# Kernel optimization log

Hardware: AMD Instinct MI355X
Metric: run time of the kernel (lower is better)

The kernel has to match this reference:

```python
import jax, jax.numpy as jnp
import numpy as np


def _sage_layer(x, neighbors, W, b):
    # x: (N, D), neighbors: (N, deg) int indices into x
    neigh_agg = x[neighbors].mean(axis=1)           # (N, D) gather + mean
    h = jnp.concatenate([x, neigh_agg], axis=-1)     # (N, 2D)
    return jax.nn.relu(h @ W + b)                    # (N, D_out)


def setup_inputs() -> dict:
    key = jax.random.key(0)
    k1, k2, k3, k4 = jax.random.split(key, 4)
    N, D, DEG = 50000, 128, 16
    x = jax.random.normal(k1, (N, D), dtype=jnp.float32)
    neighbors = jax.random.randint(k2, (N, DEG), 0, N)
    # Linear(in_dim*2, out_dim) weights, stored as (2D, D_out) for x @ W
    scale = 1.0 / np.sqrt(2 * D)
    W1 = jax.random.normal(k3, (2 * D, D), dtype=jnp.float32) * scale
    b1 = jnp.zeros((D,), dtype=jnp.float32)
    W2 = jax.random.normal(k4, (2 * D, D), dtype=jnp.float32) * scale
    b2 = jnp.zeros((D,), dtype=jnp.float32)
    return {"x": x, "neighbors": neighbors, "W1": W1, "b1": b1, "W2": W2, "b2": b2}


def reference(x, neighbors, W1, b1, W2, b2):
    h = _sage_layer(x, neighbors, W1, b1)
    h = _sage_layer(h, neighbors, W2, b2)
    return h
```

## Files before the change

kernel.cpp:

```cpp
#include <hip/hip_runtime.h>

typedef __attribute__((ext_vector_type(8))) short short8;
typedef __attribute__((ext_vector_type(4))) float f32x4;
typedef __attribute__((ext_vector_type(2))) float f32x2;

#define N_NODES 50000
#define D 128
#define DEG 16
#define K2 256
#define BM 64

static __device__ __forceinline__ unsigned short f2b(float f) {
    union { float f; unsigned int u; } v; v.f = f;
    return (unsigned short)((v.u + 0x7fffu + ((v.u >> 16) & 1u)) >> 16);
}

__global__ void prep(const float* __restrict__ x, unsigned short* __restrict__ xb,
                     const float* __restrict__ W1, const float* __restrict__ W2,
                     unsigned short* __restrict__ Wf1, unsigned short* __restrict__ Wf2) {
    int b = blockIdx.x;
    if (b < 32) {
        int o  = (b * 256 + threadIdx.x) * 4;
        int e0 = o & 7;
        int l  = (o >> 3) & 63;
        int ct = (o >> 9) & 1;
        int kk = (o >> 10) & 7;
        int w  = o >> 13;
        int n  = w * 32 + ((l & 15) << 1) + ct;
        int kb = kk * 32 + (l >> 4) * 8 + e0;
        ushort4 a, c;
        a.x = f2b(W1[(kb + 0) * D + n]);
        a.y = f2b(W1[(kb + 1) * D + n]);
        a.z = f2b(W1[(kb + 2) * D + n]);
        a.w = f2b(W1[(kb + 3) * D + n]);
        *(ushort4*)(Wf1 + o) = a;
        c.x = f2b(W2[(kb + 0) * D + n]);
        c.y = f2b(W2[(kb + 1) * D + n]);
        c.z = f2b(W2[(kb + 2) * D + n]);
        c.w = f2b(W2[(kb + 3) * D + n]);
        *(ushort4*)(Wf2 + o) = c;
    } else {
        int i = ((b - 32) * 256 + threadIdx.x) * 4;
        if (i < N_NODES * D) {
            float4 v = *(const float4*)(x + i);
            ushort4 o4;
            o4.x = f2b(v.x); o4.y = f2b(v.y); o4.z = f2b(v.z); o4.w = f2b(v.w);
            *(ushort4*)(xb + i) = o4;
        }
    }
}

template <int OUT_BF16>
__global__ __launch_bounds__(256, 3)
void sage_layer(const unsigned short* __restrict__ feat,
                const int* __restrict__ nbr,
                const unsigned short* __restrict__ wf,
                const float* __restrict__ bias,
                void* __restrict__ out)
{
    __shared__ __align__(16) unsigned short Hl[BM * 264];
    __shared__ int Nl[BM * DEG];
    const int tid  = threadIdx.x;
    const int row0 = blockIdx.x * BM;

    {
        int g = row0 * DEG + tid * 4;
        int gmax = N_NODES * DEG - 4;
        if (g > gmax) g = gmax;
        *(int4*)(Nl + tid * 4) = *(const int4*)(nbr + g);
    }
    __syncthreads();

    const char* fb = (const char*)feat;

    #pragma unroll
    for (int p = 0; p < 4; ++p) {
        int a = tid + p * 256;
        int r = a >> 4;
        int s = a & 15;
        int grow = row0 + r;
        if (grow >= N_NODES) grow = N_NODES - 1;
        unsigned sB = (unsigned)s * 16u;
        short8 self = *(const short8*)(fb + (unsigned)grow * 256u + sB);

        int4 i0 = *(const int4*)(Nl + r * 16);
        int4 i1 = *(const int4*)(Nl + r * 16 + 4);
        int4 i2 = *(const int4*)(Nl + r * 16 + 8);
        int4 i3 = *(const int4*)(Nl + r * 16 + 12);
        int ids[16] = { i0.x, i0.y, i0.z, i0.w, i1.x, i1.y, i1.z, i1.w,
                        i2.x, i2.y, i2.z, i2.w, i3.x, i3.y, i3.z, i3.w };

        short8 v[16];
        #pragma unroll
        for (int j = 0; j < 16; ++j)
            v[j] = *(const short8*)(fb + (((unsigned)ids[j]) << 8) + sB);

        f32x2 am[4];
        #pragma unroll
        for (int i = 0; i < 4; ++i) am[i] = (f32x2){0.f, 0.f};
        #pragma unroll
        for (int j = 0; j < 16; ++j) {
            union { short8 s8; unsigned u[4]; } vv; vv.s8 = v[j];
            #pragma unroll
            for (int i = 0; i < 4; ++i) {
                unsigned ui = vv.u[i];
                f32x2 e;
                e.x = __uint_as_float(ui << 16);
                e.y = __uint_as_float(ui & 0xffff0000u);
                am[i] += e;
            }
        }

        unsigned short* hr = Hl + r * 264 + s * 8;
        *(short8*)(hr) = self;
        union { unsigned short u[8]; short8 s8; } m;
        #pragma unroll
        for (int i = 0; i < 4; ++i) {
            m.u[2 * i]     = f2b(am[i].x * 0.0625f);
            m.u[2 * i + 1] = f2b(am[i].y * 0.0625f);
        }
        *(short8*)(hr + D) = m.s8;
    }

    const int lane = tid & 63;
    const int w    = tid >> 6;
    const int quad = lane >> 4;
    const int l16  = lane & 15;
    const int n_base = w * 32;
    const unsigned short* wfw = wf + w * 8192;
    short8 bfrag[8][2];
    #pragma unroll
    for (int kk = 0; kk < 8; ++kk)
        #pragma unroll
        for (int ct = 0; ct < 2; ++ct)
            bfrag[kk][ct] = *(const short8*)(wfw + kk * 1024 + ct * 512 + lane * 8);

    __syncthreads();

    f32x4 acc[4][2];
    #pragma unroll
    for (int rt = 0; rt < 4; ++rt)
        #pragma unroll
        for (int ct = 0; ct < 2; ++ct)
            acc[rt][ct] = (f32x4){0.f, 0.f, 0.f, 0.f};

    #pragma unroll
    for (int kk = 0; kk < 8; ++kk) {
        short8 afrag[4];
        #pragma unroll
        for (int rt = 0; rt < 4; ++rt)
            afrag[rt] = *(const short8*)(&Hl[(rt * 16 + l16) * 264 + kk * 32 + quad * 8]);
        #pragma unroll
        for (int rt = 0; rt < 4; ++rt)
            #pragma unroll
            for (int ct = 0; ct < 2; ++ct)
                acc[rt][ct] = __builtin_amdgcn_mfma_f32_16x16x32_bf16(
                    afrag[rt], bfrag[kk][ct], acc[rt][ct], 0, 0, 0);
    }

    const int col0 = n_base + (l16 << 1);
    float2 bv = *(const float2*)(bias + col0);
    #pragma unroll
    for (int rt = 0; rt < 4; ++rt) {
        int grow_base = row0 + rt * 16 + quad * 4;
        #pragma unroll
        for (int r = 0; r < 4; ++r) {
            int grow = grow_base + r;
            if (grow >= N_NODES) continue;
            float v0 = acc[rt][0][r] + bv.x;
            float v1 = acc[rt][1][r] + bv.y;
            v0 = v0 > 0.f ? v0 : 0.f;
            v1 = v1 > 0.f ? v1 : 0.f;
            if (OUT_BF16) {
                unsigned u = (unsigned)f2b(v0) | ((unsigned)f2b(v1) << 16);
                *(unsigned*)((unsigned short*)out + grow * D + col0) = u;
            } else {
                float2 o2; o2.x = v0; o2.y = v1;
                *(float2*)((float*)out + grow * D + col0) = o2;
            }
        }
    }
}

extern "C" void kernel_launch(void* const* d_in, const int* in_sizes, int n_in,
                              void* d_out, int out_size, void* d_ws, size_t ws_size,
                              hipStream_t stream) {
    const float* x  = (const float*)d_in[0];
    const int*   nb = (const int*)d_in[1];
    const float* W1 = (const float*)d_in[2];
    const float* b1 = (const float*)d_in[3];
    const float* W2 = (const float*)d_in[4];
    const float* b2 = (const float*)d_in[5];

    char* ws = (char*)d_ws;
    unsigned short* Wf1 = (unsigned short*)(ws);
    unsigned short* Wf2 = (unsigned short*)(ws + 65536);
    unsigned short* xb  = (unsigned short*)(ws + 131072);
    unsigned short* h1  = (unsigned short*)(ws + 131072 + 12800000);

    prep<<<32 + 6250, 256, 0, stream>>>(x, xb, W1, W2, Wf1, Wf2);

    const int mgrid = (N_NODES + BM - 1) / BM;
    sage_layer<1><<<mgrid, 256, 0, stream>>>(xb, nb, Wf1, b1, h1);
    sage_layer<0><<<mgrid, 256, 0, stream>>>(h1, nb, Wf2, b2, d_out);
}
```

Before: 147.8 us.

## Split fused SAGE layer into column-chunked gather and LDS-swizzled GEMM kernels

Stores bf16 features in a column-chunked layout: four chunks of 32 features each, one 64-byte row segment per node per chunk. Each layer is split into a separate gather-mean kernel, run with a chunk dimension in the grid so the random gathers in one pass touch a smaller working set, and a GEMM kernel. The GEMM loads A tiles straight into swizzled LDS with global_load_lds. This aims to improve cache locality of the random neighbor gathers and raise occupancy. The cost is two extra kernel launches and a round trip through global memory for the mean buffer.

```diff
diff --git a/kernel.cpp b/kernel.cpp
--- a/kernel.cpp
+++ b/kernel.cpp
@@ -8,14 +8,14 @@
 #define D 128
 #define DEG 16
 #define K2 256
-#define BM 64
+#define CHSZ (N_NODES * 64u)
 
 static __device__ __forceinline__ unsigned short f2b(float f) {
     union { float f; unsigned int u; } v; v.f = f;
     return (unsigned short)((v.u + 0x7fffu + ((v.u >> 16) & 1u)) >> 16);
 }
 
-__global__ void prep(const float* __restrict__ x, unsigned short* __restrict__ xb,
+__global__ void prep(const float* __restrict__ x, unsigned short* __restrict__ xcm,
                      const float* __restrict__ W1, const float* __restrict__ W2,
                      unsigned short* __restrict__ Wf1, unsigned short* __restrict__ Wf2) {
     int b = blockIdx.x;
@@ -40,94 +40,116 @@
         c.w = f2b(W2[(kb + 3) * D + n]);
         *(ushort4*)(Wf2 + o) = c;
     } else {
-        int i = ((b - 32) * 256 + threadIdx.x) * 4;
-        if (i < N_NODES * D) {
-            float4 v = *(const float4*)(x + i);
-            ushort4 o4;
-            o4.x = f2b(v.x); o4.y = f2b(v.y); o4.z = f2b(v.z); o4.w = f2b(v.w);
-            *(ushort4*)(xb + i) = o4;
-        }
-    }
-}
-
-template <int OUT_BF16>
-__global__ __launch_bounds__(256, 3)
-void sage_layer(const unsigned short* __restrict__ feat,
-                const int* __restrict__ nbr,
-                const unsigned short* __restrict__ wf,
-                const float* __restrict__ bias,
-                void* __restrict__ out)
+        unsigned o = ((unsigned)(b - 32) * 256u + threadIdx.x) * 16u;
+        unsigned rowidx = o >> 6;
+        unsigned c = rowidx / N_NODES;
+        unsigned n = rowidx - c * N_NODES;
+        unsigned d0 = (o & 63u) >> 1;
+        const float* src = x + n * 128 + c * 32 + d0;
+        float4 v0 = *(const float4*)src;
+        float4 v1 = *(const float4*)(src + 4);
+        union { unsigned short u[8]; short8 s8; } m;
+        m.u[0] = f2b(v0.x); m.u[1] = f2b(v0.y); m.u[2] = f2b(v0.z); m.u[3] = f2b(v0.w);
+        m.u[4] = f2b(v1.x); m.u[5] = f2b(v1.y); m.u[6] = f2b(v1.z); m.u[7] = f2b(v1.w);
+        *(short8*)((char*)xcm + o) = m.s8;
+    }
+}
+
+__global__ __launch_bounds__(256, 4)
+void gather_mean(const unsigned short* __restrict__ fcm,
+                 const int* __restrict__ nbr,
+                 unsigned short* __restrict__ Mcm)
 {
-    __shared__ __align__(16) unsigned short Hl[BM * 264];
-    __shared__ int Nl[BM * DEG];
+    __shared__ __align__(16) int Nl[1024];
     const int tid  = threadIdx.x;
-    const int row0 = blockIdx.x * BM;
-
-    {
-        int g = row0 * DEG + tid * 4;
-        int gmax = N_NODES * DEG - 4;
-        if (g > gmax) g = gmax;
-        *(int4*)(Nl + tid * 4) = *(const int4*)(nbr + g);
-    }
+    const int row0 = blockIdx.x * 64;
+    const char* base = (const char*)fcm + blockIdx.y * CHSZ;
+
+    int g = row0 * DEG + tid * 4;
+    int gmax = N_NODES * DEG - 4;
+    if (g > gmax) g = gmax;
+    *(int4*)(Nl + tid * 4) = *(const int4*)(nbr + g);
     __syncthreads();
 
-    const char* fb = (const char*)feat;
-
-    #pragma unroll
-    for (int p = 0; p < 4; ++p) {
-        int a = tid + p * 256;
-        int r = a >> 4;
-        int s = a & 15;
-        int grow = row0 + r;
-        if (grow >= N_NODES) grow = N_NODES - 1;
-        unsigned sB = (unsigned)s * 16u;
-        short8 self = *(const short8*)(fb + (unsigned)grow * 256u + sB);
-
-        int4 i0 = *(const int4*)(Nl + r * 16);
-        int4 i1 = *(const int4*)(Nl + r * 16 + 4);
-        int4 i2 = *(const int4*)(Nl + r * 16 + 8);
-        int4 i3 = *(const int4*)(Nl + r * 16 + 12);
-        int ids[16] = { i0.x, i0.y, i0.z, i0.w, i1.x, i1.y, i1.z, i1.w,
-                        i2.x, i2.y, i2.z, i2.w, i3.x, i3.y, i3.z, i3.w };
-
-        short8 v[16];
-        #pragma unroll
-        for (int j = 0; j < 16; ++j)
-            v[j] = *(const short8*)(fb + (((unsigned)ids[j]) << 8) + sB);
-
-        f32x2 am[4];
-        #pragma unroll
-        for (int i = 0; i < 4; ++i) am[i] = (f32x2){0.f, 0.f};
-        #pragma unroll
-        for (int j = 0; j < 16; ++j) {
-            union { short8 s8; unsigned u[4]; } vv; vv.s8 = v[j];
-            #pragma unroll
-            for (int i = 0; i < 4; ++i) {
-                unsigned ui = vv.u[i];
-                f32x2 e;
-                e.x = __uint_as_float(ui << 16);
-                e.y = __uint_as_float(ui & 0xffff0000u);
-                am[i] += e;
-            }
-        }
-
-        unsigned short* hr = Hl + r * 264 + s * 8;
-        *(short8*)(hr) = self;
+    const int r = tid >> 2, s = tid & 3;
+    const int grow = row0 + r;
+    const unsigned sB = (unsigned)s * 16u;
+
+    int4 i0 = *(const int4*)(Nl + r * 16);
+    int4 i1 = *(const int4*)(Nl + r * 16 + 4);
+    int4 i2 = *(const int4*)(Nl + r * 16 + 8);
+    int4 i3 = *(const int4*)(Nl + r * 16 + 12);
+    int ids[16] = { i0.x, i0.y, i0.z, i0.w, i1.x, i1.y, i1.z, i1.w,
+                    i2.x, i2.y, i2.z, i2.w, i3.x, i3.y, i3.z, i3.w };
+
+    short8 v[16];
+    #pragma unroll
+    for (int j = 0; j < 16; ++j)
+        v[j] = *(const short8*)(base + (((unsigned)ids[j]) << 6) + sB);
+
+    f32x2 am[4];
+    #pragma unroll
+    for (int i = 0; i < 4; ++i) am[i] = (f32x2){0.f, 0.f};
+    #pragma unroll
+    for (int j = 0; j < 16; ++j) {
+        union { short8 s8; unsigned u[4]; } vv; vv.s8 = v[j];
+        #pragma unroll
+        for (int i = 0; i < 4; ++i) {
+            unsigned ui = vv.u[i];
+            f32x2 e;
+            e.x = __uint_as_float(ui << 16);
+            e.y = __uint_as_float(ui & 0xffff0000u);
+            am[i] += e;
+        }
+    }
+
+    if (grow < N_NODES) {
         union { unsigned short u[8]; short8 s8; } m;
         #pragma unroll
         for (int i = 0; i < 4; ++i) {
             m.u[2 * i]     = f2b(am[i].x * 0.0625f);
             m.u[2 * i + 1] = f2b(am[i].y * 0.0625f);
         }
-        *(short8*)(hr + D) = m.s8;
-    }
-
+        *(short8*)((char*)Mcm + blockIdx.y * CHSZ + (unsigned)grow * 64u + sB) = m.s8;
+    }
+}
+
+template <int OUT_F32>
+__global__ __launch_bounds__(256, 4)
+void gemm(const unsigned short* __restrict__ fcm,
+          const unsigned short* __restrict__ Mcm,
+          const unsigned short* __restrict__ wf,
+          const float* __restrict__ bias,
+          void* __restrict__ out)
+{
+    __shared__ __align__(16) char Al[32 * 512];
+    const int tid  = threadIdx.x;
+    const int row0 = blockIdx.x * 32;
+    const int wave = tid >> 6;
     const int lane = tid & 63;
-    const int w    = tid >> 6;
     const int quad = lane >> 4;
     const int l16  = lane & 15;
-    const int n_base = w * 32;
-    const unsigned short* wfw = wf + w * 8192;
+
+    #pragma unroll
+    for (int i = 0; i < 4; ++i) {
+        unsigned o    = (unsigned)i * 4096u + (unsigned)tid * 16u;
+        unsigned row  = o >> 9;
+        unsigned colb = o & 511u;
+        unsigned scol = colb ^ ((row & 7u) << 4);
+        int grow = row0 + (int)row;
+        if (grow >= N_NODES) grow = N_NODES - 1;
+        const unsigned short* buf = (scol < 256u) ? fcm : Mcm;
+        unsigned cb = scol & 255u;
+        const char* src = (const char*)buf + (cb >> 6) * CHSZ
+                          + (unsigned)grow * 64u + (cb & 63u);
+        __builtin_amdgcn_global_load_lds(
+            (const __attribute__((address_space(1))) unsigned int*)src,
+            (__attribute__((address_space(3))) unsigned int*)
+                (Al + i * 4096 + wave * 1024),
+            16, 0, 0);
+    }
+
+    const unsigned short* wfw = wf + wave * 8192;
     short8 bfrag[8][2];
     #pragma unroll
     for (int kk = 0; kk < 8; ++kk)
@@ -137,46 +159,51 @@
 
     __syncthreads();
 
-    f32x4 acc[4][2];
-    #pragma unroll
-    for (int rt = 0; rt < 4; ++rt)
+    f32x4 acc[2][2];
+    #pragma unroll
+    for (int rt = 0; rt < 2; ++rt)
         #pragma unroll
         for (int ct = 0; ct < 2; ++ct)
             acc[rt][ct] = (f32x4){0.f, 0.f, 0.f, 0.f};
 
     #pragma unroll
     for (int kk = 0; kk < 8; ++kk) {
-        short8 afrag[4];
-        #pragma unroll
-        for (int rt = 0; rt < 4; ++rt)
-            afrag[rt] = *(const short8*)(&Hl[(rt * 16 + l16) * 264 + kk * 32 + quad * 8]);
-        #pragma unroll
-        for (int rt = 0; rt < 4; ++rt)
+        short8 af[2];
+        #pragma unroll
+        for (int rt = 0; rt < 2; ++rt) {
+            unsigned row  = (unsigned)(rt * 16 + l16);
+            unsigned byte = row * 512u + (unsigned)kk * 64u + (unsigned)quad * 16u;
+            byte ^= (row & 7u) << 4;
+            af[rt] = *(const short8*)(Al + byte);
+        }
+        #pragma unroll
+        for (int rt = 0; rt < 2; ++rt)
             #pragma unroll
             for (int ct = 0; ct < 2; ++ct)
                 acc[rt][ct] = __builtin_amdgcn_mfma_f32_16x16x32_bf16(
-                    afrag[rt], bfrag[kk][ct], acc[rt][ct], 0, 0, 0);
-    }
-
-    const int col0 = n_base + (l16 << 1);
+                    af[rt], bfrag[kk][ct], acc[rt][ct], 0, 0, 0);
+    }
+
+    const int col0 = wave * 32 + (l16 << 1);
     float2 bv = *(const float2*)(bias + col0);
     #pragma unroll
-    for (int rt = 0; rt < 4; ++rt) {
-        int grow_base = row0 + rt * 16 + quad * 4;
+    for (int rt = 0; rt < 2; ++rt) {
+        int gb = row0 + rt * 16 + quad * 4;
         #pragma unroll
         for (int r = 0; r < 4; ++r) {
-            int grow = grow_base + r;
+            int grow = gb + r;
             if (grow >= N_NODES) continue;
             float v0 = acc[rt][0][r] + bv.x;
             float v1 = acc[rt][1][r] + bv.y;
             v0 = v0 > 0.f ? v0 : 0.f;
             v1 = v1 > 0.f ? v1 : 0.f;
-            if (OUT_BF16) {
+            if (OUT_F32) {
+                f32x2 o2; o2.x = v0; o2.y = v1;
+                *(f32x2*)((float*)out + grow * D + col0) = o2;
+            } else {
                 unsigned u = (unsigned)f2b(v0) | ((unsigned)f2b(v1) << 16);
-                *(unsigned*)((unsigned short*)out + grow * D + col0) = u;
-            } else {
-                float2 o2; o2.x = v0; o2.y = v1;
-                *(float2*)((float*)out + grow * D + col0) = o2;
+                *(unsigned*)((char*)out + (col0 >> 5) * CHSZ
+                             + (unsigned)grow * 64u + (col0 & 31) * 2) = u;
             }
         }
     }
@@ -193,14 +220,19 @@
     const float* b2 = (const float*)d_in[5];
 
     char* ws = (char*)d_ws;
-    unsigned short* Wf1 = (unsigned short*)(ws);
-    unsigned short* Wf2 = (unsigned short*)(ws + 65536);
-    unsigned short* xb  = (unsigned short*)(ws + 131072);
-    unsigned short* h1  = (unsigned short*)(ws + 131072 + 12800000);
-
-    prep<<<32 + 6250, 256, 0, stream>>>(x, xb, W1, W2, Wf1, Wf2);
-
-    const int mgrid = (N_NODES + BM - 1) / BM;
-    sage_layer<1><<<mgrid, 256, 0, stream>>>(xb, nb, Wf1, b1, h1);
-    sage_layer<0><<<mgrid, 256, 0, stream>>>(h1, nb, Wf2, b2, d_out);
-}
+    unsigned short* Wf1  = (unsigned short*)(ws);
+    unsigned short* Wf2  = (unsigned short*)(ws + 65536);
+    unsigned short* xcm  = (unsigned short*)(ws + 131072);
+    unsigned short* Mcm  = (unsigned short*)(ws + 131072 + 12800000);
+    unsigned short* h1cm = (unsigned short*)(ws + 131072 + 25600000);
+
+    prep<<<32 + 3125, 256, 0, stream>>>(x, xcm, W1, W2, Wf1, Wf2);
+
+    const int ggrid = (N_NODES + 63) / 64;
+    const int mgrid = (N_NODES + 31) / 32;
+
+    gather_mean<<<dim3(ggrid, 4), 256, 0, stream>>>(xcm, nb, Mcm);
+    gemm<0><<<mgrid, 256, 0, stream>>>(xcm, Mcm, Wf1, b1, h1cm);
+    gather_mean<<<dim3(ggrid, 4), 256, 0, stream>>>(h1cm, nb, Mcm);
+    gemm<1><<<mgrid, 256, 0, stream>>>(h1cm, Mcm, Wf2, b2, d_out);
+}
```

Result: slower. 177.5 us (+20.1%).

## Gather neighbor features from an FP8 copy and halve the row tile

Applied to the files above, without the earlier changes.

Writes an extra FP8 (e4m3) copy of the input features and of the layer-1 output, and does the 16-neighbor gather from those 8-byte chunks instead of 16-byte bf16 chunks. This halves the bytes moved by the random-access gather. The row tile also drops from 64 to 32 rows and the occupancy hint rises from 3 to 4 blocks, which doubles the grid. The cost is extra prep and epilogue writes, plus a much coarser neighbor mean from FP8 quantization that could exceed the accuracy tolerance.

```diff
diff --git a/kernel.cpp b/kernel.cpp
--- a/kernel.cpp
+++ b/kernel.cpp
@@ -7,8 +7,7 @@
 #define N_NODES 50000
 #define D 128
 #define DEG 16
-#define K2 256
-#define BM 64
+#define BM 32
 
 static __device__ __forceinline__ unsigned short f2b(float f) {
     union { float f; unsigned int u; } v; v.f = f;
@@ -16,6 +15,7 @@
 }
 
 __global__ void prep(const float* __restrict__ x, unsigned short* __restrict__ xb,
+                     unsigned char* __restrict__ xq,
                      const float* __restrict__ W1, const float* __restrict__ W2,
                      unsigned short* __restrict__ Wf1, unsigned short* __restrict__ Wf2) {
     int b = blockIdx.x;
@@ -46,24 +46,29 @@
             ushort4 o4;
             o4.x = f2b(v.x); o4.y = f2b(v.y); o4.z = f2b(v.z); o4.w = f2b(v.w);
             *(ushort4*)(xb + i) = o4;
+            int q = __builtin_amdgcn_cvt_pk_fp8_f32(v.x, v.y, 0, false);
+            q = __builtin_amdgcn_cvt_pk_fp8_f32(v.z, v.w, q, true);
+            *(unsigned*)(xq + i) = (unsigned)q;
         }
     }
 }
 
 template <int OUT_BF16>
-__global__ __launch_bounds__(256, 3)
+__global__ __launch_bounds__(256, 4)
 void sage_layer(const unsigned short* __restrict__ feat,
+                const unsigned char* __restrict__ featq,
                 const int* __restrict__ nbr,
                 const unsigned short* __restrict__ wf,
                 const float* __restrict__ bias,
-                void* __restrict__ out)
+                void* __restrict__ out,
+                unsigned char* __restrict__ outq)
 {
     __shared__ __align__(16) unsigned short Hl[BM * 264];
     __shared__ int Nl[BM * DEG];
     const int tid  = threadIdx.x;
     const int row0 = blockIdx.x * BM;
 
-    {
+    if (tid < 128) {
         int g = row0 * DEG + tid * 4;
         int gmax = N_NODES * DEG - 4;
         if (g > gmax) g = gmax;
@@ -72,16 +77,16 @@
     __syncthreads();
 
     const char* fb = (const char*)feat;
-
-    #pragma unroll
-    for (int p = 0; p < 4; ++p) {
+    const char* qb = (const char*)featq;
+
+    #pragma unroll
+    for (int p = 0; p < 2; ++p) {
         int a = tid + p * 256;
         int r = a >> 4;
         int s = a & 15;
         int grow = row0 + r;
         if (grow >= N_NODES) grow = N_NODES - 1;
-        unsigned sB = (unsigned)s * 16u;
-        short8 self = *(const short8*)(fb + (unsigned)grow * 256u + sB);
+        short8 self = *(const short8*)(fb + (unsigned)grow * 256u + (unsigned)s * 16u);
 
         int4 i0 = *(const int4*)(Nl + r * 16);
         int4 i1 = *(const int4*)(Nl + r * 16 + 4);
@@ -90,25 +95,20 @@
         int ids[16] = { i0.x, i0.y, i0.z, i0.w, i1.x, i1.y, i1.z, i1.w,
                         i2.x, i2.y, i2.z, i2.w, i3.x, i3.y, i3.z, i3.w };
 
-        short8 v[16];
+        uint2 v[16];
         #pragma unroll
         for (int j = 0; j < 16; ++j)
-            v[j] = *(const short8*)(fb + (((unsigned)ids[j]) << 8) + sB);
+            v[j] = *(const uint2*)(qb + (((unsigned)ids[j]) << 7) + (unsigned)s * 8u);
 
         f32x2 am[4];
         #pragma unroll
         for (int i = 0; i < 4; ++i) am[i] = (f32x2){0.f, 0.f};
         #pragma unroll
         for (int j = 0; j < 16; ++j) {
-            union { short8 s8; unsigned u[4]; } vv; vv.s8 = v[j];
-            #pragma unroll
-            for (int i = 0; i < 4; ++i) {
-                unsigned ui = vv.u[i];
-                f32x2 e;
-                e.x = __uint_as_float(ui << 16);
-                e.y = __uint_as_float(ui & 0xffff0000u);
-                am[i] += e;
-            }
+            am[0] += __builtin_amdgcn_cvt_pk_f32_fp8(v[j].x, false);
+            am[1] += __builtin_amdgcn_cvt_pk_f32_fp8(v[j].x, true);
+            am[2] += __builtin_amdgcn_cvt_pk_f32_fp8(v[j].y, false);
+            am[3] += __builtin_amdgcn_cvt_pk_f32_fp8(v[j].y, true);
         }
 
         unsigned short* hr = Hl + r * 264 + s * 8;
@@ -126,7 +126,6 @@
     const int w    = tid >> 6;
     const int quad = lane >> 4;
     const int l16  = lane & 15;
-    const int n_base = w * 32;
     const unsigned short* wfw = wf + w * 8192;
     short8 bfrag[8][2];
     #pragma unroll
@@ -137,35 +136,35 @@
 
     __syncthreads();
 
-    f32x4 acc[4][2];
-    #pragma unroll
-    for (int rt = 0; rt < 4; ++rt)
+    f32x4 acc[2][2];
+    #pragma unroll
+    for (int rt = 0; rt < 2; ++rt)
         #pragma unroll
         for (int ct = 0; ct < 2; ++ct)
             acc[rt][ct] = (f32x4){0.f, 0.f, 0.f, 0.f};
 
     #pragma unroll
     for (int kk = 0; kk < 8; ++kk) {
-        short8 afrag[4];
-        #pragma unroll
-        for (int rt = 0; rt < 4; ++rt)
-            afrag[rt] = *(const short8*)(&Hl[(rt * 16 + l16) * 264 + kk * 32 + quad * 8]);
-        #pragma unroll
-        for (int rt = 0; rt < 4; ++rt)
+        short8 af[2];
+        #pragma unroll
+        for (int rt = 0; rt < 2; ++rt)
+            af[rt] = *(const short8*)(&Hl[(rt * 16 + l16) * 264 + kk * 32 + quad * 8]);
+        #pragma unroll
+        for (int rt = 0; rt < 2; ++rt)
             #pragma unroll
             for (int ct = 0; ct < 2; ++ct)
                 acc[rt][ct] = __builtin_amdgcn_mfma_f32_16x16x32_bf16(
-                    afrag[rt], bfrag[kk][ct], acc[rt][ct], 0, 0, 0);
-    }
-
-    const int col0 = n_base + (l16 << 1);
+                    af[rt], bfrag[kk][ct], acc[rt][ct], 0, 0, 0);
+    }
+
+    const int col0 = w * 32 + (l16 << 1);
     float2 bv = *(const float2*)(bias + col0);
     #pragma unroll
-    for (int rt = 0; rt < 4; ++rt) {
-        int grow_base = row0 + rt * 16 + quad * 4;
+    for (int rt = 0; rt < 2; ++rt) {
+        int gb = row0 + rt * 16 + quad * 4;
         #pragma unroll
         for (int r = 0; r < 4; ++r) {
-            int grow = grow_base + r;
+            int grow = gb + r;
             if (grow >= N_NODES) continue;
             float v0 = acc[rt][0][r] + bv.x;
             float v1 = acc[rt][1][r] + bv.y;
@@ -174,9 +173,11 @@
             if (OUT_BF16) {
                 unsigned u = (unsigned)f2b(v0) | ((unsigned)f2b(v1) << 16);
                 *(unsigned*)((unsigned short*)out + grow * D + col0) = u;
+                int q = __builtin_amdgcn_cvt_pk_fp8_f32(v0, v1, 0, false);
+                *(unsigned short*)(outq + grow * D + col0) = (unsigned short)q;
             } else {
-                float2 o2; o2.x = v0; o2.y = v1;
-                *(float2*)((float*)out + grow * D + col0) = o2;
+                f32x2 o2; o2.x = v0; o2.y = v1;
+                *(f32x2*)((float*)out + grow * D + col0) = o2;
             }
         }
     }
@@ -197,10 +198,12 @@
     unsigned short* Wf2 = (unsigned short*)(ws + 65536);
     unsigned short* xb  = (unsigned short*)(ws + 131072);
     unsigned short* h1  = (unsigned short*)(ws + 131072 + 12800000);
-
-    prep<<<32 + 6250, 256, 0, stream>>>(x, xb, W1, W2, Wf1, Wf2);
+    unsigned char*  xq  = (unsigned char*)(ws + 131072 + 25600000);
+    unsigned char*  h1q = (unsigned char*)(ws + 131072 + 32000000);
+
+    prep<<<32 + 6250, 256, 0, stream>>>(x, xb, xq, W1, W2, Wf1, Wf2);
 
     const int mgrid = (N_NODES + BM - 1) / BM;
-    sage_layer<1><<<mgrid, 256, 0, stream>>>(xb, nb, Wf1, b1, h1);
-    sage_layer<0><<<mgrid, 256, 0, stream>>>(h1, nb, Wf2, b2, d_out);
-}
+    sage_layer<1><<<mgrid, 256, 0, stream>>>(xb, xq, nb, Wf1, b1, h1, h1q);
+    sage_layer<0><<<mgrid, 256, 0, stream>>>(h1, h1q, nb, Wf2, b2, d_out, nullptr);
+}
```

Result: faster. 124.9 us (-15.5%).
